# Kernel tuning notes

Measured on AMD Instinct MI355X. Metric: run time of the kernel, lower is better.

## Reference

```python
import jax, jax.numpy as jnp
import numpy as np

KERNELS = (2, 4, 8, 16, 32)
DICE_EPS = 1e-6
WEIGHT = 1.0


def _projections(x):
    # x: [B, D, H, W] foreground volume. Three axis-max projections, each [B, 128, 128].
    return jnp.stack([x.max(axis=3),   # axial:    max over W -> [B, D, H]
                      x.max(axis=1),   # sagittal: max over D -> [B, H, W]
                      x.max(axis=2)],  # coronal:  max over H -> [B, D, W]
                     axis=0)           # [3, B, S, S] with S = 128


def _maxpool2d(x, k):
    # x: [3, B, S, S], non-overlapping max pool with kernel=stride=k (k divides S)
    t, b, s, _ = x.shape
    return x.reshape(t, b, s // k, k, s // k, k).max(axis=(3, 5))


def setup_inputs() -> dict:
    key = jax.random.key(0)
    k1, k2 = jax.random.split(key)
    shape = (8, 2, 128, 128, 128)
    inp = jax.random.uniform(k1, shape, dtype=jnp.float32)
    tgt = jax.random.uniform(k2, shape, dtype=jnp.float32)
    return {"input": inp, "target": tgt}


def reference(input, target):
    yh = input[:, 1]   # [B, D, H, W] foreground prediction
    yt = target[:, 1]  # [B, D, H, W] foreground target

    # ---- multi-scale topology loss ----
    P = _projections(yh)  # [3, B, 128, 128]
    G = _projections(yt)
    losses = []
    for k in KERNELS:
        Pk = _maxpool2d(P, k).sum(axis=0)  # [B, 128/k, 128/k]
        Gk = _maxpool2d(G, k).sum(axis=0)
        losses.append(jnp.abs(Gk - Pk).mean())
    topo_loss = jnp.mean(jnp.stack(losses))

    # ---- dice loss (foreground channel, squared denominator) ----
    b = yh.shape[0]
    a = yh.reshape(b, -1)
    t = yt.reshape(b, -1)
    intersection = jnp.sum(a * t, axis=1)
    denom = jnp.sum(a * a, axis=1) + jnp.sum(t * t, axis=1)
    dice_coeff = (2.0 * intersection + DICE_EPS) / denom
    dice_loss = 1.0 - dice_coeff.mean()

    return WEIGHT * topo_loss + WEIGHT * dice_loss
```

## Files before the change

### kernel.cpp

```cpp
#include <hip/hip_runtime.h>

#define S 128
#define SS (S*S)
#define B 8
#define BSS (B*SS)
#define NEG_INF (-3.402823466e+38f)

#define ACC_LOSS 0
#define ACC_DICE 8
#define PA   1024
#define PBP  (PA  + 2*BSS)
#define PCP  (PBP + 2*8*8*SS)

__device__ __forceinline__ float4 max4(float4 a, float4 b) {
  return make_float4(fmaxf(a.x,b.x), fmaxf(a.y,b.y), fmaxf(a.z,b.z), fmaxf(a.w,b.w));
}
__device__ __forceinline__ float hmax4(float4 a) {
  return fmaxf(fmaxf(a.x,a.y), fmaxf(a.z,a.w));
}
__device__ __forceinline__ float4 shflx4(float4 v, int m) {
  return make_float4(__shfl_xor(v.x,m,64), __shfl_xor(v.y,m,64),
                     __shfl_xor(v.z,m,64), __shfl_xor(v.w,m,64));
}

__global__ __launch_bounds__(1024, 4) void proj_dice_kernel(
    const float* __restrict__ gin, const float* __restrict__ gtg,
    float* __restrict__ ws)
{
  const int jc  = blockIdx.x;
  const int ic  = blockIdx.y;
  const int b   = blockIdx.z;
  const int tid = threadIdx.x;
  const int jr  = tid >> 5;
  const int kl  = tid & 31;
  const int j   = (jc << 5) + jr;
  const int i0  = ic << 4;
  const int k0  = kl << 2;
  const int w   = tid >> 6;
  const int h   = (tid >> 5) & 1;

  const float* __restrict__ xin = gin + (size_t)(2*b + 1) * (size_t)(S*SS);
  const float* __restrict__ xtg = gtg + (size_t)(2*b + 1) * (size_t)(S*SS);

  float* paI = ws + PA + (size_t)(0*B + b)*SS;
  float* paT = ws + PA + (size_t)(1*B + b)*SS;
  float* pbI = ws + PBP + (size_t)((0*B + b)*8 + ic)*SS;
  float* pbT = ws + PBP + (size_t)((1*B + b)*8 + ic)*SS;
  float* pcI = ws + PCP + (size_t)((0*B + b)*4 + jc)*SS;
  float* pcT = ws + PCP + (size_t)((1*B + b)*4 + jc)*SS;

  __shared__ float lpc[2][4][2][16][S];
  __shared__ float dred[16][3];

  float4 pba = make_float4(NEG_INF, NEG_INF, NEG_INF, NEG_INF);
  float4 pbt = pba;
  float s_at = 0.f, s_aa = 0.f, s_tt = 0.f;

  for (int r = 0; r < 4; ++r) {
    const int par = r & 1;
    #pragma unroll
    for (int q = 0; q < 4; ++q) {
      const int i = i0 + (r << 2) + q;
      const size_t off = (size_t)i*SS + (size_t)j*S + k0;
      const float4 a = *(const float4*)(xin + off);
      const float4 t = *(const float4*)(xtg + off);

      s_at = fmaf(a.x,t.x, fmaf(a.y,t.y, fmaf(a.z,t.z, fmaf(a.w,t.w, s_at))));
      s_aa = fmaf(a.x,a.x, fmaf(a.y,a.y, fmaf(a.z,a.z, fmaf(a.w,a.w, s_aa))));
      s_tt = fmaf(t.x,t.x, fmaf(t.y,t.y, fmaf(t.z,t.z, fmaf(t.w,t.w, s_tt))));

      pba = max4(pba, a);
      pbt = max4(pbt, t);

      float rma = hmax4(a), rmt = hmax4(t);
      #pragma unroll
      for (int m = 16; m >= 1; m >>= 1) {
        rma = fmaxf(rma, __shfl_xor(rma, m, 64));
        rmt = fmaxf(rmt, __shfl_xor(rmt, m, 64));
      }
      if (kl == 0) { paI[i*S + j] = rma; paT[i*S + j] = rmt; }

      const float4 pca = max4(a, shflx4(a, 32));
      const float4 pct = max4(t, shflx4(t, 32));
      if (h == 0) {
        *(float4*)&lpc[par][q][0][w][k0] = pca;
        *(float4*)&lpc[par][q][1][w][k0] = pct;
      }
    }
    __syncthreads();
    {
      const int q  = tid >> 8;
      const int t  = (tid >> 7) & 1;
      const int k  = tid & 127;
      float m = lpc[par][q][t][0][k];
      #pragma unroll
      for (int rr = 1; rr < 16; ++rr) m = fmaxf(m, lpc[par][q][t][rr][k]);
      const int i = i0 + (r << 2) + q;
      (t ? pcT : pcI)[i*S + k] = m;
    }
  }

  *(float4*)(pbI + j*S + k0) = pba;
  *(float4*)(pbT + j*S + k0) = pbt;

  float v0 = s_at, v1 = s_aa, v2 = s_tt;
  #pragma unroll
  for (int m = 32; m >= 1; m >>= 1) {
    v0 += __shfl_xor(v0, m, 64);
    v1 += __shfl_xor(v1, m, 64);
    v2 += __shfl_xor(v2, m, 64);
  }
  if ((tid & 63) == 0) { dred[w][0] = v0; dred[w][1] = v1; dred[w][2] = v2; }
  __syncthreads();
  if (tid == 0) {
    float a0 = 0.f, a1 = 0.f, a2 = 0.f;
    #pragma unroll
    for (int rr = 0; rr < 16; ++rr) { a0 += dred[rr][0]; a1 += dred[rr][1]; a2 += dred[rr][2]; }
    const int bid = jc + 4*ic + 32*b;
    ws[ACC_DICE + bid*3 + 0] = a0;
    ws[ACC_DICE + bid*3 + 1] = a1;
    ws[ACC_DICE + bid*3 + 2] = a2;
  }
}

__global__ __launch_bounds__(256) void pool_loss_kernel(float* __restrict__ ws)
{
  const int b   = blockIdx.x;
  const int tid = threadIdx.x;
  const int tr  = tid >> 4;
  const int tc  = tid & 15;
  const int r0  = tr << 3;
  const int c0  = tc << 3;

  float s2[2][4][4];
  float s4[2][2][2];
  float s8[2], s16[2], s32[2];
  #pragma unroll
  for (int v = 0; v < 2; ++v) {
    #pragma unroll
    for (int y = 0; y < 4; ++y)
      #pragma unroll
      for (int x = 0; x < 4; ++x) s2[v][y][x] = 0.f;
    #pragma unroll
    for (int y = 0; y < 2; ++y)
      #pragma unroll
      for (int x = 0; x < 2; ++x) s4[v][y][x] = 0.f;
    s8[v] = 0.f; s16[v] = 0.f; s32[v] = 0.f;
  }

  #pragma unroll
  for (int t = 0; t < 3; ++t) {
    #pragma unroll
    for (int vol = 0; vol < 2; ++vol) {
      const int np = (t == 0) ? 1 : (t == 1) ? 8 : 4;
      const float* base =
        (t == 0) ? ws + PA  + (size_t)(vol*B + b)*SS :
        (t == 1) ? ws + PBP + (size_t)((vol*B + b)*8)*SS :
                   ws + PCP + (size_t)((vol*B + b)*4)*SS;
      float tile[8][8];
      #pragma unroll
      for (int r = 0; r < 8; ++r)
        #pragma unroll
        for (int c = 0; c < 8; ++c) tile[r][c] = NEG_INF;
      for (int p = 0; p < np; ++p) {
        const float* m = base + (size_t)p*SS;
        #pragma unroll
        for (int r = 0; r < 8; ++r) {
          const float4 a = *(const float4*)(m + (size_t)(r0 + r)*S + c0);
          const float4 c = *(const float4*)(m + (size_t)(r0 + r)*S + c0 + 4);
          tile[r][0]=fmaxf(tile[r][0],a.x); tile[r][1]=fmaxf(tile[r][1],a.y);
          tile[r][2]=fmaxf(tile[r][2],a.z); tile[r][3]=fmaxf(tile[r][3],a.w);
          tile[r][4]=fmaxf(tile[r][4],c.x); tile[r][5]=fmaxf(tile[r][5],c.y);
          tile[r][6]=fmaxf(tile[r][6],c.z); tile[r][7]=fmaxf(tile[r][7],c.w);
        }
      }
      float m2[4][4];
      #pragma unroll
      for (int y = 0; y < 4; ++y)
        #pragma unroll
        for (int x = 0; x < 4; ++x) {
          m2[y][x] = fmaxf(fmaxf(tile[2*y][2*x], tile[2*y][2*x+1]),
                           fmaxf(tile[2*y+1][2*x], tile[2*y+1][2*x+1]));
          s2[vol][y][x] += m2[y][x];
        }
      float m4[2][2];
      #pragma unroll
      for (int y = 0; y < 2; ++y)
        #pragma unroll
        for (int x = 0; x < 2; ++x) {
          m4[y][x] = fmaxf(fmaxf(m2[2*y][2*x], m2[2*y][2*x+1]),
                           fmaxf(m2[2*y+1][2*x], m2[2*y+1][2*x+1]));
          s4[vol][y][x] += m4[y][x];
        }
      float m8 = fmaxf(fmaxf(m4[0][0], m4[0][1]), fmaxf(m4[1][0], m4[1][1]));
      s8[vol] += m8;
      float m16 = m8;
      m16 = fmaxf(m16, __shfl_xor(m16, 1, 64));
      m16 = fmaxf(m16, __shfl_xor(m16, 16, 64));
      s16[vol] += m16;
      float m32 = m16;
      m32 = fmaxf(m32, __shfl_xor(m32, 2, 64));
      m32 = fmaxf(m32, __shfl_xor(m32, 32, 64));
      s32[vol] += m32;
    }
  }

  const float w0 = 1.f/(5.f*8.f*64.f*64.f);
  const float w1 = 1.f/(5.f*8.f*32.f*32.f);
  const float w2 = 1.f/(5.f*8.f*16.f*16.f);
  const float w3 = 1.f/(5.f*8.f*8.f*8.f);
  const float w4 = 1.f/(5.f*8.f*4.f*4.f);

  float l0 = 0.f;
  #pragma unroll
  for (int y = 0; y < 4; ++y)
    #pragma unroll
    for (int x = 0; x < 4; ++x) l0 += fabsf(s2[1][y][x] - s2[0][y][x]);
  float l1 = 0.f;
  #pragma unroll
  for (int y = 0; y < 2; ++y)
    #pragma unroll
    for (int x = 0; x < 2; ++x) l1 += fabsf(s4[1][y][x] - s4[0][y][x]);
  float part = l0*w0 + l1*w1 + fabsf(s8[1] - s8[0])*w2;
  if ((tid & 0x11) == 0) part += fabsf(s16[1] - s16[0])*w3;
  if ((tid & 0x33) == 0) part += fabsf(s32[1] - s32[0])*w4;

  #pragma unroll
  for (int m = 32; m >= 1; m >>= 1) part += __shfl_xor(part, m, 64);
  __shared__ float red[4];
  const int wid = tid >> 6;
  if ((tid & 63) == 0) red[wid] = part;
  __syncthreads();
  if (tid == 0) ws[ACC_LOSS + b] = red[0] + red[1] + red[2] + red[3];
}

__global__ __launch_bounds__(256) void finalize_kernel(
    const float* __restrict__ ws, float* __restrict__ out)
{
  const int tid = threadIdx.x;
  __shared__ float fd[8];

  float v0 = ws[ACC_DICE + tid*3 + 0];
  float v1 = ws[ACC_DICE + tid*3 + 1];
  float v2 = ws[ACC_DICE + tid*3 + 2];
  #pragma unroll
  for (int m = 16; m >= 1; m >>= 1) {
    v0 += __shfl_xor(v0, m, 64);
    v1 += __shfl_xor(v1, m, 64);
    v2 += __shfl_xor(v2, m, 64);
  }
  if ((tid & 31) == 0) fd[tid >> 5] = (2.f*v0 + 1e-6f) / (v1 + v2);
  __syncthreads();
  if (tid == 0) {
    float topo = 0.f, dsum = 0.f;
    #pragma unroll
    for (int b = 0; b < B; ++b) { topo += ws[ACC_LOSS + b]; dsum += fd[b]; }
    out[0] = topo + (1.f - dsum / (float)B);
  }
}

extern "C" void kernel_launch(void* const* d_in, const int* in_sizes, int n_in,
                              void* d_out, int out_size, void* d_ws, size_t ws_size,
                              hipStream_t stream)
{
  const float* gin = (const float*)d_in[0];
  const float* gtg = (const float*)d_in[1];
  float* ws  = (float*)d_ws;
  float* out = (float*)d_out;

  dim3 g1(4, 8, B);
  proj_dice_kernel<<<g1, dim3(1024), 0, stream>>>(gin, gtg, ws);

  pool_loss_kernel<<<B, dim3(256), 0, stream>>>(ws);

  finalize_kernel<<<1, dim3(256), 0, stream>>>(ws, out);
}
```

Before: 51.76 us.

## Reduce coronal partial maxima via shared-memory atomicMax and coalesce axial stores

Coronal projection partials are now folded into one shared buffer with integer atomicMax, using an order-preserving float-to-uint mapping. This replaces the per-round double-buffered staging, the per-round __syncthreads and the 16-way serial reduction. Axial row maxima are staged in shared memory and written out once as coalesced stores instead of scattered per-lane global writes. In exchange it adds many LDS atomics, which can contend because 16 waves hit the same addresses, and it shrinks shared memory use, which may allow higher occupancy.

```diff
diff --git a/kernel.cpp b/kernel.cpp
--- a/kernel.cpp
+++ b/kernel.cpp
@@ -12,6 +12,15 @@
 #define PBP  (PA  + 2*BSS)
 #define PCP  (PBP + 2*8*8*SS)
 
+#define MAPF_NEGMAX 0x00800000u
+
+__device__ __forceinline__ unsigned mapf(float f) {
+  unsigned u = __float_as_uint(f);
+  return (u & 0x80000000u) ? ~u : (u | 0x80000000u);
+}
+__device__ __forceinline__ float unmapf(unsigned u) {
+  return (u & 0x80000000u) ? __uint_as_float(u & 0x7FFFFFFFu) : __uint_as_float(~u);
+}
 __device__ __forceinline__ float4 max4(float4 a, float4 b) {
   return make_float4(fmaxf(a.x,b.x), fmaxf(a.y,b.y), fmaxf(a.z,b.z), fmaxf(a.w,b.w));
 }
@@ -49,18 +58,25 @@
   float* pcI = ws + PCP + (size_t)((0*B + b)*4 + jc)*SS;
   float* pcT = ws + PCP + (size_t)((1*B + b)*4 + jc)*SS;
 
-  __shared__ float lpc[2][4][2][16][S];
-  __shared__ float dred[16][3];
+  __shared__ unsigned lpc[2][16][S];
+  __shared__ float    lpa[2][16][32];
+  __shared__ float    dred[16][3];
+
+  {
+    unsigned* p = &lpc[0][0][0] + tid*4;
+    p[0] = MAPF_NEGMAX; p[1] = MAPF_NEGMAX; p[2] = MAPF_NEGMAX; p[3] = MAPF_NEGMAX;
+  }
+  __syncthreads();
 
   float4 pba = make_float4(NEG_INF, NEG_INF, NEG_INF, NEG_INF);
   float4 pbt = pba;
   float s_at = 0.f, s_aa = 0.f, s_tt = 0.f;
 
   for (int r = 0; r < 4; ++r) {
-    const int par = r & 1;
     #pragma unroll
     for (int q = 0; q < 4; ++q) {
-      const int i = i0 + (r << 2) + q;
+      const int ii = (r << 2) + q;
+      const int i  = i0 + ii;
       const size_t off = (size_t)i*SS + (size_t)j*S + k0;
       const float4 a = *(const float4*)(xin + off);
       const float4 t = *(const float4*)(xtg + off);
@@ -78,26 +94,38 @@
         rma = fmaxf(rma, __shfl_xor(rma, m, 64));
         rmt = fmaxf(rmt, __shfl_xor(rmt, m, 64));
       }
-      if (kl == 0) { paI[i*S + j] = rma; paT[i*S + j] = rmt; }
+      if (kl == 0) { lpa[0][ii][jr] = rma; lpa[1][ii][jr] = rmt; }
 
       const float4 pca = max4(a, shflx4(a, 32));
       const float4 pct = max4(t, shflx4(t, 32));
       if (h == 0) {
-        *(float4*)&lpc[par][q][0][w][k0] = pca;
-        *(float4*)&lpc[par][q][1][w][k0] = pct;
+        atomicMax(&lpc[0][ii][k0+0], mapf(pca.x));
+        atomicMax(&lpc[0][ii][k0+1], mapf(pca.y));
+        atomicMax(&lpc[0][ii][k0+2], mapf(pca.z));
+        atomicMax(&lpc[0][ii][k0+3], mapf(pca.w));
+        atomicMax(&lpc[1][ii][k0+0], mapf(pct.x));
+        atomicMax(&lpc[1][ii][k0+1], mapf(pct.y));
+        atomicMax(&lpc[1][ii][k0+2], mapf(pct.z));
+        atomicMax(&lpc[1][ii][k0+3], mapf(pct.w));
       }
     }
-    __syncthreads();
-    {
-      const int q  = tid >> 8;
-      const int t  = (tid >> 7) & 1;
-      const int k  = tid & 127;
-      float m = lpc[par][q][t][0][k];
-      #pragma unroll
-      for (int rr = 1; rr < 16; ++rr) m = fmaxf(m, lpc[par][q][t][rr][k]);
-      const int i = i0 + (r << 2) + q;
-      (t ? pcT : pcI)[i*S + k] = m;
-    }
+  }
+
+  __syncthreads();
+
+  {
+    const int t  = tid >> 9;
+    const int ii = (tid >> 5) & 15;
+    const int kq = (tid & 31) << 2;
+    const float4 v = make_float4(unmapf(lpc[t][ii][kq+0]), unmapf(lpc[t][ii][kq+1]),
+                                 unmapf(lpc[t][ii][kq+2]), unmapf(lpc[t][ii][kq+3]));
+    *(float4*)((t ? pcT : pcI) + (size_t)(i0+ii)*S + kq) = v;
+  }
+  {
+    const int t  = tid >> 9;
+    const int ii = (tid >> 5) & 15;
+    const int jj = tid & 31;
+    (t ? paT : paI)[(size_t)(i0+ii)*S + (jc << 5) + jj] = lpa[t][ii][jj];
   }
 
   *(float4*)(pbI + j*S + k0) = pba;
```

Measured after the change: 52.95 us. 1.02x slower.

## Fuse finalize into pool kernel via last-block atomic and split pool work in halves

Applied to the files above, without the earlier changes.

Removes the separate finalize kernel launch. The pool_loss kernel now uses a global atomic counter, reset by the first block of the projection kernel, so the last-finishing block computes the final dice and topology reduction. Each batch's pooling work is also split across two 128-thread blocks by column half, doubling the block count, with the shuffle masks adjusted to the new lane layout. This saves one launch and its gap, at the cost of an atomic and a serialized tail in one block.

```diff
diff --git a/kernel.cpp b/kernel.cpp
--- a/kernel.cpp
+++ b/kernel.cpp
@@ -7,7 +7,8 @@
 #define NEG_INF (-3.402823466e+38f)
 
 #define ACC_LOSS 0
-#define ACC_DICE 8
+#define ACC_DICE 16
+#define ACC_CNT  1008
 #define PA   1024
 #define PBP  (PA  + 2*BSS)
 #define PCP  (PBP + 2*8*8*SS)
@@ -39,6 +40,9 @@
   const int w   = tid >> 6;
   const int h   = (tid >> 5) & 1;
 
+  if (tid == 0 && jc == 0 && ic == 0 && b == 0)
+    ((unsigned*)ws)[ACC_CNT] = 0u;
+
   const float* __restrict__ xin = gin + (size_t)(2*b + 1) * (size_t)(S*SS);
   const float* __restrict__ xtg = gtg + (size_t)(2*b + 1) * (size_t)(S*SS);
 
@@ -123,14 +127,16 @@
   }
 }
 
-__global__ __launch_bounds__(256) void pool_loss_kernel(float* __restrict__ ws)
+__global__ __launch_bounds__(128) void pool_loss_kernel(
+    float* __restrict__ ws, float* __restrict__ out)
 {
-  const int b   = blockIdx.x;
-  const int tid = threadIdx.x;
-  const int tr  = tid >> 4;
-  const int tc  = tid & 15;
-  const int r0  = tr << 3;
-  const int c0  = tc << 3;
+  const int half = blockIdx.x;
+  const int b    = blockIdx.y;
+  const int tid  = threadIdx.x;
+  const int tr   = tid >> 3;
+  const int tc   = tid & 7;
+  const int r0   = tr << 3;
+  const int c0   = (half << 6) + (tc << 3);
 
   float s2[2][4][4];
   float s4[2][2][2];
@@ -196,11 +202,11 @@
       s8[vol] += m8;
       float m16 = m8;
       m16 = fmaxf(m16, __shfl_xor(m16, 1, 64));
-      m16 = fmaxf(m16, __shfl_xor(m16, 16, 64));
+      m16 = fmaxf(m16, __shfl_xor(m16, 8, 64));
       s16[vol] += m16;
       float m32 = m16;
       m32 = fmaxf(m32, __shfl_xor(m32, 2, 64));
-      m32 = fmaxf(m32, __shfl_xor(m32, 32, 64));
+      m32 = fmaxf(m32, __shfl_xor(m32, 16, 64));
       s32[vol] += m32;
     }
   }
@@ -222,39 +228,48 @@
     #pragma unroll
     for (int x = 0; x < 2; ++x) l1 += fabsf(s4[1][y][x] - s4[0][y][x]);
   float part = l0*w0 + l1*w1 + fabsf(s8[1] - s8[0])*w2;
-  if ((tid & 0x11) == 0) part += fabsf(s16[1] - s16[0])*w3;
-  if ((tid & 0x33) == 0) part += fabsf(s32[1] - s32[0])*w4;
+  if ((tid & 0x09) == 0) part += fabsf(s16[1] - s16[0])*w3;
+  if ((tid & 0x1B) == 0) part += fabsf(s32[1] - s32[0])*w4;
 
   #pragma unroll
   for (int m = 32; m >= 1; m >>= 1) part += __shfl_xor(part, m, 64);
-  __shared__ float red[4];
-  const int wid = tid >> 6;
-  if ((tid & 63) == 0) red[wid] = part;
-  __syncthreads();
-  if (tid == 0) ws[ACC_LOSS + b] = red[0] + red[1] + red[2] + red[3];
-}
-
-__global__ __launch_bounds__(256) void finalize_kernel(
-    const float* __restrict__ ws, float* __restrict__ out)
-{
-  const int tid = threadIdx.x;
+  __shared__ float red[2];
+  __shared__ int   isLast;
+  if ((tid & 63) == 0) red[tid >> 6] = part;
+  __syncthreads();
+  if (tid == 0) {
+    ws[ACC_LOSS + (b << 1) + half] = red[0] + red[1];
+    unsigned old = __hip_atomic_fetch_add((unsigned*)ws + ACC_CNT, 1u,
+                                          __ATOMIC_ACQ_REL,
+                                          __HIP_MEMORY_SCOPE_AGENT);
+    isLast = (old == 15u);
+  }
+  __syncthreads();
+  if (!isLast) return;
+
   __shared__ float fd[8];
-
-  float v0 = ws[ACC_DICE + tid*3 + 0];
-  float v1 = ws[ACC_DICE + tid*3 + 1];
-  float v2 = ws[ACC_DICE + tid*3 + 2];
-  #pragma unroll
-  for (int m = 16; m >= 1; m >>= 1) {
-    v0 += __shfl_xor(v0, m, 64);
-    v1 += __shfl_xor(v1, m, 64);
-    v2 += __shfl_xor(v2, m, 64);
-  }
-  if ((tid & 31) == 0) fd[tid >> 5] = (2.f*v0 + 1e-6f) / (v1 + v2);
+  {
+    const int bf = tid >> 4;
+    const int g  = tid & 15;
+    const int bid = (bf << 5) + (g << 1);
+    float v0 = ws[ACC_DICE + bid*3 + 0] + ws[ACC_DICE + (bid+1)*3 + 0];
+    float v1 = ws[ACC_DICE + bid*3 + 1] + ws[ACC_DICE + (bid+1)*3 + 1];
+    float v2 = ws[ACC_DICE + bid*3 + 2] + ws[ACC_DICE + (bid+1)*3 + 2];
+    #pragma unroll
+    for (int m = 8; m >= 1; m >>= 1) {
+      v0 += __shfl_xor(v0, m, 64);
+      v1 += __shfl_xor(v1, m, 64);
+      v2 += __shfl_xor(v2, m, 64);
+    }
+    if (g == 0) fd[bf] = (2.f*v0 + 1e-6f) / (v1 + v2);
+  }
   __syncthreads();
   if (tid == 0) {
     float topo = 0.f, dsum = 0.f;
     #pragma unroll
-    for (int b = 0; b < B; ++b) { topo += ws[ACC_LOSS + b]; dsum += fd[b]; }
+    for (int x = 0; x < 16; ++x) topo += ws[ACC_LOSS + x];
+    #pragma unroll
+    for (int bb = 0; bb < B; ++bb) dsum += fd[bb];
     out[0] = topo + (1.f - dsum / (float)B);
   }
 }
@@ -271,7 +286,5 @@
   dim3 g1(4, 8, B);
   proj_dice_kernel<<<g1, dim3(1024), 0, stream>>>(gin, gtg, ws);
 
-  pool_loss_kernel<<<B, dim3(256), 0, stream>>>(ws);
-
-  finalize_kernel<<<1, dim3(256), 0, stream>>>(ws, out);
-}
+  pool_loss_kernel<<<dim3(2, B), dim3(128), 0, stream>>>(ws, out);
+}
```

New measurement: 43.55 us. 15.9% less time.
